# Optimization experiments

Hardware: AMD Instinct MI355X
Metric: run time of the kernel (lower is better)

Reference implementation:

```python
import jax, jax.numpy as jnp
import numpy as np

N = 8192
IN_F = 512
OUT_F = 128
NUM_CLASSES = 10
ALPHA = 0.2  # LeakyReLU negative slope
NEG_INF = -9e15


def setup_inputs() -> dict:
    key = jax.random.key(0)
    k_h, k_d, k_W, k_a, k_cw, k_cb = jax.random.split(key, 6)
    h = jax.random.normal(k_h, (N, IN_F), dtype=jnp.float32)
    dist = jax.random.randint(k_d, (N, N), 0, 2, dtype=jnp.int32)
    # xavier_uniform with gain=1.414
    gain = 1.414
    lim_W = gain * np.sqrt(6.0 / (IN_F + OUT_F))
    W = jax.random.uniform(k_W, (IN_F, OUT_F), minval=-lim_W, maxval=lim_W, dtype=jnp.float32)
    lim_a = gain * np.sqrt(6.0 / (2 * OUT_F + 1))
    a = jax.random.uniform(k_a, (2 * OUT_F, 1), minval=-lim_a, maxval=lim_a, dtype=jnp.float32)
    # nn.Linear(out_features, num_classes): weight [C, out], bias [C]
    lim_c = np.sqrt(1.0 / OUT_F)
    Wc = jax.random.uniform(k_cw, (NUM_CLASSES, OUT_F), minval=-lim_c, maxval=lim_c, dtype=jnp.float32)
    bc = jax.random.uniform(k_cb, (NUM_CLASSES,), minval=-lim_c, maxval=lim_c, dtype=jnp.float32)
    return {"h": h, "dist": dist, "W": W, "a": a, "Wc": Wc, "bc": bc}


def reference(h, dist, W, a, Wc, bc):
    Wh = h @ W                              # [N, out]
    Wh1 = Wh @ a[:OUT_F]                    # [N, 1]
    Wh2 = Wh @ a[OUT_F:]                    # [N, 1]
    e = jax.nn.leaky_relu(Wh1 + Wh2.T, negative_slope=ALPHA)  # [N, N]
    att = jnp.where(dist > 0, e, NEG_INF)
    att = jax.nn.softmax(att, axis=1)       # [N, N]
    h_update = jax.nn.elu(att @ Wh)         # [N, out] (dropout inactive at inference)
    y_pred = h_update @ Wc.T + bc           # [N, num_classes]
    return y_pred
```

## Files before the change

### kernel.cpp

```cpp
#include <hip/hip_runtime.h>
#include <stdint.h>

#define N 8192
#define IN_F 512
#define OUT_F 128
#define NCLS 10
#define ALPHA 0.2f

typedef float f32x4 __attribute__((ext_vector_type(4)));
typedef int   i32x4 __attribute__((ext_vector_type(4)));
typedef short s16x4 __attribute__((ext_vector_type(4)));
typedef short s16x8 __attribute__((ext_vector_type(8)));

__device__ __forceinline__ short f2bf(float x) {
    unsigned u = __builtin_bit_cast(unsigned, x);
    u = (u + 0x7FFFu + ((u >> 16) & 1u)) >> 16;
    return (short)u;
}
__device__ __forceinline__ float bf2f(short s) {
    unsigned u = ((unsigned)(unsigned short)s) << 16;
    return __builtin_bit_cast(float, u);
}

__global__ __launch_bounds__(256, 8)
void mask_kernel(const int* __restrict__ dist, unsigned* __restrict__ mask) {
    size_t w = (size_t)blockIdx.x * 256 + threadIdx.x;
    const int* p = dist + w * 32;
    unsigned b = 0;
    #pragma unroll
    for (int u = 0; u < 8; ++u) {
        i32x4 v = *(const i32x4*)(p + u * 4);
        #pragma unroll
        for (int e = 0; e < 4; ++e) b |= (v[e] > 0 ? 1u : 0u) << (u * 4 + e);
    }
    mask[w] = b;
}

__global__ void split_w_kernel(const float* __restrict__ W,
                               short* __restrict__ WThi, short* __restrict__ WTlo) {
    int idx = blockIdx.x * 256 + threadIdx.x;
    int k = idx >> 7, col = idx & 127;
    float x = W[idx];
    short hi = f2bf(x);
    short lo = f2bf(x - bf2f(hi));
    size_t a = (size_t)(k >> 5) * (128 * 32) + (size_t)col * 32 + (k & 31);
    WThi[a] = hi;
    WTlo[a] = lo;
}

#define WH_ROWS 16
#define WH_STR 520

__global__ __launch_bounds__(256, 2)
void wh_kernel(const float* __restrict__ h, const short* __restrict__ WThi,
               const short* __restrict__ WTlo, const float* __restrict__ a,
               short* __restrict__ WhT, float* __restrict__ Wh1,
               float* __restrict__ Wh2) {
    __shared__ __align__(16) short Ahi[WH_ROWS][WH_STR];
    __shared__ __align__(16) short Alo[WH_ROWS][WH_STR];
    __shared__ __align__(16) float whs[WH_ROWS][OUT_F + 4];

    const int t = threadIdx.x;
    const int r0 = blockIdx.x * WH_ROWS;

    {
        int row = t >> 4, c4 = t & 15;
        const float* hrow = h + (size_t)(r0 + row) * IN_F;
        #pragma unroll
        for (int jj = 0; jj < 4; ++jj) {
            int k0 = c4 * 8 + jj * 128;
            f32x4 x0 = *(const f32x4*)(hrow + k0);
            f32x4 x1 = *(const f32x4*)(hrow + k0 + 4);
            s16x8 hi, lo;
            #pragma unroll
            for (int e = 0; e < 4; ++e) {
                short h0 = f2bf(x0[e]); hi[e] = h0; lo[e] = f2bf(x0[e] - bf2f(h0));
                short h1 = f2bf(x1[e]); hi[4 + e] = h1; lo[4 + e] = f2bf(x1[e] - bf2f(h1));
            }
            *(s16x8*)&Ahi[row][k0] = hi;
            *(s16x8*)&Alo[row][k0] = lo;
        }
    }
    __syncthreads();

    const int lane = t & 63, w = t >> 6;
    const int q = lane >> 4, ln16 = lane & 15;
    f32x4 acc[2] = {};
    #pragma unroll
    for (int kc = 0; kc < IN_F / 32; ++kc) {
        s16x8 ahi = *(const s16x8*)&Ahi[ln16][kc * 32 + q * 8];
        s16x8 alo = *(const s16x8*)&Alo[ln16][kc * 32 + q * 8];
        #pragma unroll
        for (int nt = 0; nt < 2; ++nt) {
            int col = w * 32 + nt * 16 + ln16;
            size_t boff = (size_t)kc * 4096 + (size_t)col * 32 + q * 8;
            s16x8 bhi = *(const s16x8*)(WThi + boff);
            s16x8 blo = *(const s16x8*)(WTlo + boff);
            acc[nt] = __builtin_amdgcn_mfma_f32_16x16x32_bf16(ahi, bhi, acc[nt], 0, 0, 0);
            acc[nt] = __builtin_amdgcn_mfma_f32_16x16x32_bf16(ahi, blo, acc[nt], 0, 0, 0);
            acc[nt] = __builtin_amdgcn_mfma_f32_16x16x32_bf16(alo, bhi, acc[nt], 0, 0, 0);
        }
    }
    #pragma unroll
    for (int nt = 0; nt < 2; ++nt)
        #pragma unroll
        for (int reg = 0; reg < 4; ++reg)
            whs[q * 4 + reg][w * 32 + nt * 16 + ln16] = acc[nt][reg];
    __syncthreads();

    if (t < 128) {
        int r = t >> 3, s = t & 7;
        float s1 = 0.f, s2 = 0.f;
        #pragma unroll
        for (int cc = 0; cc < 16; ++cc) {
            int c = s * 16 + cc;
            float v = whs[r][c];
            s1 = fmaf(v, a[c], s1);
            s2 = fmaf(v, a[OUT_F + c], s2);
        }
        s1 += __shfl_xor(s1, 1); s1 += __shfl_xor(s1, 2); s1 += __shfl_xor(s1, 4);
        s2 += __shfl_xor(s2, 1); s2 += __shfl_xor(s2, 2); s2 += __shfl_xor(s2, 4);
        if (s == 0) { Wh1[r0 + r] = s1; Wh2[r0 + r] = s2; }
    }

    {
        int c = t >> 1, h8 = t & 1;
        s16x8 pack;
        #pragma unroll
        for (int rr = 0; rr < 8; ++rr) pack[rr] = f2bf(whs[h8 * 8 + rr][c]);
        size_t addr = (size_t)(r0 >> 5) * 4096 + (size_t)c * 32 + (r0 & 16) + h8 * 8;
        *(s16x8*)(WhT + addr) = pack;
    }
}

#define BM 32
#define BK 128
#define ASTR (BK + 8)
#define SPLIT 4
#define NIT (N / (BK * SPLIT))
#define JSPAN (N / SPLIT)

__global__ __launch_bounds__(256, 6)
void attn_kernel(const unsigned* __restrict__ mask, const short* __restrict__ WhT,
                 const float* __restrict__ Wh1v, const float* __restrict__ Wh2v,
                 float* __restrict__ acc_part, float* __restrict__ l_part) {
    __shared__ __align__(16) short As[2][BM][ASTR];
    __shared__ __align__(16) float wh2s[JSPAN];

    const int t = threadIdx.x;
    const int it = blockIdx.x & 255;
    const int sp = blockIdx.x >> 8;
    const int i0 = it * BM;
    const int r = t >> 3, s = t & 7;
    const int lane = t & 63, w = t >> 6;
    const int q = lane >> 4, ln16 = lane & 15;
    const int j0 = sp * JSPAN;
    const int sh = s * 4;

    {
        f32x4 a0 = *(const f32x4*)(Wh2v + j0 + t * 8);
        f32x4 a1 = *(const f32x4*)(Wh2v + j0 + t * 8 + 4);
        *(f32x4*)&wh2s[t * 8] = a0;
        *(f32x4*)&wh2s[t * 8 + 4] = a1;
    }

    const unsigned* __restrict__ mrow = mask + (size_t)(i0 + r) * (N / 32) + (j0 >> 5);
    const float wh1 = Wh1v[i0 + r];
    float l_acc = 0.f;
    f32x4 acc[2][2] = {};

    i32x4 m = *(const i32x4*)mrow;
    __syncthreads();

    for (int kt = 0; kt < NIT; ++kt) {
        const int jb = kt * BK;
        i32x4 mn = m;
        if (kt + 1 < NIT) mn = *(const i32x4*)(mrow + (kt + 1) * 4);
        short* arow = &As[kt & 1][r][0];
        #pragma unroll
        for (int u = 0; u < 4; ++u) {
            f32x4 w2 = *(const f32x4*)&wh2s[jb + u * 32 + sh];
            unsigned nib = ((unsigned)m[u] >> sh) & 15u;
            s16x4 pk;
            #pragma unroll
            for (int e = 0; e < 4; ++e) {
                float sv = wh1 + w2[e];
                float lr = fmaxf(sv, ALPHA * sv);
                float pv = (nib & (1u << e)) ? __expf(lr) : 0.f;
                l_acc += pv;
                pk[e] = f2bf(pv);
            }
            *(s16x4*)(arow + u * 32 + sh) = pk;
        }
        __syncthreads();
        const short* ab = &As[kt & 1][0][0];
        const short* bbase = WhT + (size_t)(j0 + jb) * 128;
        #pragma unroll
        for (int kc = 0; kc < BK / 32; ++kc) {
            s16x8 a0 = *(const s16x8*)(ab + ln16 * ASTR + kc * 32 + q * 8);
            s16x8 a1 = *(const s16x8*)(ab + (16 + ln16) * ASTR + kc * 32 + q * 8);
            #pragma unroll
            for (int nt = 0; nt < 2; ++nt) {
                int col = w * 32 + nt * 16 + ln16;
                s16x8 b = *(const s16x8*)(bbase + (size_t)kc * 4096 + col * 32 + q * 8);
                acc[0][nt] = __builtin_amdgcn_mfma_f32_16x16x32_bf16(a0, b, acc[0][nt], 0, 0, 0);
                acc[1][nt] = __builtin_amdgcn_mfma_f32_16x16x32_bf16(a1, b, acc[1][nt], 0, 0, 0);
            }
        }
        m = mn;
    }

    l_acc += __shfl_xor(l_acc, 1);
    l_acc += __shfl_xor(l_acc, 2);
    l_acc += __shfl_xor(l_acc, 4);
    if (s == 0) l_part[(size_t)sp * N + i0 + r] = l_acc;

    float* ap = acc_part + (size_t)sp * N * OUT_F + (size_t)i0 * OUT_F;
    #pragma unroll
    for (int mt = 0; mt < 2; ++mt)
        #pragma unroll
        for (int reg = 0; reg < 4; ++reg) {
            int row = mt * 16 + q * 4 + reg;
            #pragma unroll
            for (int nt = 0; nt < 2; ++nt)
                ap[(size_t)row * OUT_F + w * 32 + nt * 16 + ln16] = acc[mt][nt][reg];
        }
}

__global__ __launch_bounds__(256, 4)
void reduce_kernel(const float* __restrict__ acc_part, const float* __restrict__ l_part,
                   const float* __restrict__ Wc, const float* __restrict__ bcv,
                   float* __restrict__ out, int split) {
    __shared__ __align__(16) float hu[16][OUT_F + 4];
    const int t = threadIdx.x;
    const int i0 = blockIdx.x * 16;
    const int row = t >> 4, cg = t & 15;

    f32x4 v0 = {0.f, 0.f, 0.f, 0.f}, v1 = {0.f, 0.f, 0.f, 0.f};
    float l = 0.f;
    for (int s = 0; s < split; ++s) {
        const float* ap = acc_part + (size_t)s * N * OUT_F + (size_t)(i0 + row) * OUT_F + cg * 8;
        v0 += *(const f32x4*)ap;
        v1 += *(const f32x4*)(ap + 4);
        l += l_part[(size_t)s * N + i0 + row];
    }
    float inv = 1.f / l;
    #pragma unroll
    for (int e = 0; e < 4; ++e) {
        float x0 = v0[e] * inv; x0 = x0 > 0.f ? x0 : (__expf(x0) - 1.f);
        float x1 = v1[e] * inv; x1 = x1 > 0.f ? x1 : (__expf(x1) - 1.f);
        hu[row][cg * 8 + e] = x0;
        hu[row][cg * 8 + 4 + e] = x1;
    }
    __syncthreads();

    if (t < 16 * NCLS) {
        int rr = t / NCLS, cls = t - rr * NCLS;
        const f32x4* hurow = (const f32x4*)&hu[rr][0];
        const f32x4* wcrow = (const f32x4*)(Wc + cls * OUT_F);
        float sum = bcv[cls];
        #pragma unroll 8
        for (int c4 = 0; c4 < OUT_F / 4; ++c4) {
            f32x4 hv = hurow[c4];
            f32x4 wv = wcrow[c4];
            sum += hv[0] * wv[0] + hv[1] * wv[1] + hv[2] * wv[2] + hv[3] * wv[3];
        }
        out[(size_t)(i0 + rr) * NCLS + cls] = sum;
    }
}

extern "C" void kernel_launch(void* const* d_in, const int* in_sizes, int n_in,
                              void* d_out, int out_size, void* d_ws, size_t ws_size,
                              hipStream_t stream) {
    const float* h    = (const float*)d_in[0];
    const int*   dist = (const int*)d_in[1];
    const float* W    = (const float*)d_in[2];
    const float* a    = (const float*)d_in[3];
    const float* Wc   = (const float*)d_in[4];
    const float* bc   = (const float*)d_in[5];
    float* out = (float*)d_out;

    char* ws = (char*)d_ws;
    size_t off = 0;
    short* WhT  = (short*)(ws + off); off += (size_t)OUT_F * N * 2;
    short* WThi = (short*)(ws + off); off += (size_t)IN_F * OUT_F * 2;
    short* WTlo = (short*)(ws + off); off += (size_t)IN_F * OUT_F * 2;
    float* Wh1  = (float*)(ws + off); off += (size_t)N * 4;
    float* Wh2  = (float*)(ws + off); off += (size_t)N * 4;
    unsigned* mask = (unsigned*)(ws + off); off += (size_t)N * (N / 32) * 4;

    float* acc_part = (float*)(ws + off); off += (size_t)SPLIT * N * OUT_F * 4;
    float* l_part   = (float*)(ws + off);

    hipLaunchKernelGGL(mask_kernel, dim3(N * (N / 32) / 256), dim3(256), 0, stream,
                       dist, mask);
    hipLaunchKernelGGL(split_w_kernel, dim3(256), dim3(256), 0, stream, W, WThi, WTlo);
    hipLaunchKernelGGL(wh_kernel, dim3(N / WH_ROWS), dim3(256), 0, stream,
                       h, WThi, WTlo, a, WhT, Wh1, Wh2);
    hipLaunchKernelGGL(attn_kernel, dim3(256 * SPLIT), dim3(256), 0, stream,
                       mask, WhT, Wh1, Wh2, acc_part, l_part);
    hipLaunchKernelGGL(reduce_kernel, dim3(N / 16), dim3(256), 0, stream,
                       acc_part, l_part, Wc, bc, out, SPLIT);
}
```

Measured before the change: 443.4 us.

## Double BK, prefetch Wh2 and mask into registers, ping-pong attention pipeline

Doubles the K tile to 256 and drops the shared-memory copy of Wh2. Wh2 values and mask words are now loaded straight from global memory into two register buffers, so the next tile's loads are issued before the current tile's MFMA phase. The loop is unrolled by two, alternating the LDS buffers explicitly, and the occupancy hint drops from 6 to 4 blocks per CU. This aims to hide global load latency behind compute and halve the loop iterations. The cost is higher register pressure and lower occupancy.

```diff
diff --git a/kernel.cpp b/kernel.cpp
--- a/kernel.cpp
+++ b/kernel.cpp
@@ -134,18 +134,58 @@
 }
 
 #define BM 32
-#define BK 128
+#define BK 256
 #define ASTR (BK + 8)
 #define SPLIT 4
 #define NIT (N / (BK * SPLIT))
-#define JSPAN (N / SPLIT)
-
-__global__ __launch_bounds__(256, 6)
+
+__device__ __forceinline__ f32x4 mfma16(s16x8 a, s16x8 b, f32x4 c) {
+    return __builtin_amdgcn_mfma_f32_16x16x32_bf16(a, b, c, 0, 0, 0);
+}
+
+__device__ __forceinline__ void pphase(const f32x4 (&wb)[8], i32x4 m0, i32x4 m1,
+                                       short* arow, int sh, float wh1,
+                                       float& l_acc) {
+    #pragma unroll
+    for (int u = 0; u < 8; ++u) {
+        f32x4 w2 = wb[u];
+        unsigned wrd = (unsigned)((u < 4) ? m0[u] : m1[u - 4]);
+        unsigned nib = (wrd >> sh) & 15u;
+        s16x4 pk;
+        #pragma unroll
+        for (int e = 0; e < 4; ++e) {
+            float sv = wh1 + w2[e];
+            float lr = fmaxf(sv, ALPHA * sv);
+            float pv = (nib & (1u << e)) ? __expf(lr) : 0.f;
+            l_acc += pv;
+            pk[e] = f2bf(pv);
+        }
+        *(s16x4*)(arow + u * 32 + sh) = pk;
+    }
+}
+
+__device__ __forceinline__ void mfmaphase(const short* ab, const short* bbase,
+                                          int ln16, int q, int w,
+                                          f32x4 (&acc)[2][2]) {
+    #pragma unroll
+    for (int kc = 0; kc < BK / 32; ++kc) {
+        s16x8 a0 = *(const s16x8*)(ab + ln16 * ASTR + kc * 32 + q * 8);
+        s16x8 a1 = *(const s16x8*)(ab + (16 + ln16) * ASTR + kc * 32 + q * 8);
+        #pragma unroll
+        for (int nt = 0; nt < 2; ++nt) {
+            int col = w * 32 + nt * 16 + ln16;
+            s16x8 b = *(const s16x8*)(bbase + (size_t)kc * 4096 + col * 32 + q * 8);
+            acc[0][nt] = mfma16(a0, b, acc[0][nt]);
+            acc[1][nt] = mfma16(a1, b, acc[1][nt]);
+        }
+    }
+}
+
+__global__ __launch_bounds__(256, 4)
 void attn_kernel(const unsigned* __restrict__ mask, const short* __restrict__ WhT,
                  const float* __restrict__ Wh1v, const float* __restrict__ Wh2v,
                  float* __restrict__ acc_part, float* __restrict__ l_part) {
     __shared__ __align__(16) short As[2][BM][ASTR];
-    __shared__ __align__(16) float wh2s[JSPAN];
 
     const int t = threadIdx.x;
     const int it = blockIdx.x & 255;
@@ -154,60 +194,47 @@
     const int r = t >> 3, s = t & 7;
     const int lane = t & 63, w = t >> 6;
     const int q = lane >> 4, ln16 = lane & 15;
-    const int j0 = sp * JSPAN;
+    const int j0 = sp * (NIT * BK);
     const int sh = s * 4;
 
-    {
-        f32x4 a0 = *(const f32x4*)(Wh2v + j0 + t * 8);
-        f32x4 a1 = *(const f32x4*)(Wh2v + j0 + t * 8 + 4);
-        *(f32x4*)&wh2s[t * 8] = a0;
-        *(f32x4*)&wh2s[t * 8 + 4] = a1;
-    }
-
     const unsigned* __restrict__ mrow = mask + (size_t)(i0 + r) * (N / 32) + (j0 >> 5);
+    const float* __restrict__ wh2p = Wh2v + j0 + sh;
     const float wh1 = Wh1v[i0 + r];
     float l_acc = 0.f;
     f32x4 acc[2][2] = {};
 
-    i32x4 m = *(const i32x4*)mrow;
-    __syncthreads();
-
-    for (int kt = 0; kt < NIT; ++kt) {
-        const int jb = kt * BK;
-        i32x4 mn = m;
-        if (kt + 1 < NIT) mn = *(const i32x4*)(mrow + (kt + 1) * 4);
-        short* arow = &As[kt & 1][r][0];
-        #pragma unroll
-        for (int u = 0; u < 4; ++u) {
-            f32x4 w2 = *(const f32x4*)&wh2s[jb + u * 32 + sh];
-            unsigned nib = ((unsigned)m[u] >> sh) & 15u;
-            s16x4 pk;
+    f32x4 wbA[8], wbB[8];
+    i32x4 mA0, mA1, mB0, mB1;
+
+    #pragma unroll
+    for (int u = 0; u < 8; ++u) wbA[u] = *(const f32x4*)(wh2p + u * 32);
+    mA0 = *(const i32x4*)(mrow);
+    mA1 = *(const i32x4*)(mrow + 4);
+
+    #pragma unroll
+    for (int kt2 = 0; kt2 < NIT / 2; ++kt2) {
+        const int kt = 2 * kt2;
+        pphase(wbA, mA0, mA1, &As[0][r][0], sh, wh1, l_acc);
+        {
             #pragma unroll
-            for (int e = 0; e < 4; ++e) {
-                float sv = wh1 + w2[e];
-                float lr = fmaxf(sv, ALPHA * sv);
-                float pv = (nib & (1u << e)) ? __expf(lr) : 0.f;
-                l_acc += pv;
-                pk[e] = f2bf(pv);
-            }
-            *(s16x4*)(arow + u * 32 + sh) = pk;
+            for (int u = 0; u < 8; ++u)
+                wbB[u] = *(const f32x4*)(wh2p + (kt + 1) * BK + u * 32);
+            mB0 = *(const i32x4*)(mrow + (kt + 1) * 8);
+            mB1 = *(const i32x4*)(mrow + (kt + 1) * 8 + 4);
         }
         __syncthreads();
-        const short* ab = &As[kt & 1][0][0];
-        const short* bbase = WhT + (size_t)(j0 + jb) * 128;
-        #pragma unroll
-        for (int kc = 0; kc < BK / 32; ++kc) {
-            s16x8 a0 = *(const s16x8*)(ab + ln16 * ASTR + kc * 32 + q * 8);
-            s16x8 a1 = *(const s16x8*)(ab + (16 + ln16) * ASTR + kc * 32 + q * 8);
+        mfmaphase(&As[0][0][0], WhT + (size_t)(j0 + kt * BK) * 128, ln16, q, w, acc);
+
+        pphase(wbB, mB0, mB1, &As[1][r][0], sh, wh1, l_acc);
+        if (kt2 + 1 < NIT / 2) {
             #pragma unroll
-            for (int nt = 0; nt < 2; ++nt) {
-                int col = w * 32 + nt * 16 + ln16;
-                s16x8 b = *(const s16x8*)(bbase + (size_t)kc * 4096 + col * 32 + q * 8);
-                acc[0][nt] = __builtin_amdgcn_mfma_f32_16x16x32_bf16(a0, b, acc[0][nt], 0, 0, 0);
-                acc[1][nt] = __builtin_amdgcn_mfma_f32_16x16x32_bf16(a1, b, acc[1][nt], 0, 0, 0);
-            }
-        }
-        m = mn;
+            for (int u = 0; u < 8; ++u)
+                wbA[u] = *(const f32x4*)(wh2p + (kt + 2) * BK + u * 32);
+            mA0 = *(const i32x4*)(mrow + (kt + 2) * 8);
+            mA1 = *(const i32x4*)(mrow + (kt + 2) * 8 + 4);
+        }
+        __syncthreads();
+        mfmaphase(&As[1][0][0], WhT + (size_t)(j0 + (kt + 1) * BK) * 128, ln16, q, w, acc);
     }
 
     l_acc += __shfl_xor(l_acc, 1);
```

Result: no change. 444.4 us (+0.2%).
